# Performance work log

Hardware: AMD Instinct MI355X
Metric: run time of the kernel (lower is better)

Reference implementation:

```python
import jax, jax.numpy as jnp
import numpy as np

N = 100000      # nodes
E = 3200000     # edges (avg degree 32)
DIN = 128       # in_channels
DH = 256        # hidden == out_channels


def _xavier(key, fan_in, fan_out):
    s = float(np.sqrt(2.0 / (fan_in + fan_out)))
    return jax.random.normal(key, (fan_in, fan_out), dtype=jnp.float32) * s


def setup_inputs() -> dict:
    key = jax.random.key(0)
    ks = jax.random.split(key, 16)
    x = jax.random.normal(ks[0], (N, DIN), dtype=jnp.float32)
    edge_index = jax.random.randint(ks[1], (2, E), 0, N, dtype=jnp.int32)
    inp = {"x": x, "edge_index": edge_index}
    dims = [(DIN, DH), (DH, DH), (DH, DH), (DH, DH), (DH, DH), (DH, DH)]
    names = [("w11", "b11"), ("w12", "b12"), ("w21", "b21"), ("w22", "b22"), ("w31", "b31"), ("w32", "b32")]
    for i, ((di, do), (wn, bn)) in enumerate(zip(dims, names)):
        inp[wn] = _xavier(ks[2 + i], di, do)
        inp[bn] = jnp.zeros((do,), dtype=jnp.float32)
    return inp


def reference(x, edge_index, w11, b11, w12, b12, w21, b21, w22, b22, w31, b31, w32, b32):
    src, dst = edge_index[0], edge_index[1]

    def gin_conv(h, w1, b1, w2, b2):
        # sum-aggregate neighbor features: agg[i] = sum_{(j->i) in E} h[j]
        agg = jax.ops.segment_sum(h[src], dst, num_segments=N)
        h2 = h + agg                      # (1 + eps) * x + agg, eps = 0
        h2 = jax.nn.relu(h2 @ w1 + b1)    # mlp layer 1
        return h2 @ w2 + b2               # mlp layer 2 (no activation)

    h = jax.nn.relu(gin_conv(x, w11, b11, w12, b12))
    h = jax.nn.relu(gin_conv(h, w21, b21, w22, b22))
    return gin_conv(h, w31, b31, w32, b32)
```

## Files before the change

kernel.cpp:

```cpp
#include <hip/hip_runtime.h>
#include <hip/hip_bf16.h>
#include <hip/hip_fp16.h>


#define DIN 128
#define DH  256
#define BM  256
#define BN  128
#define BK  64

#define BSHIFT 9
#define BNODES 512
#define MAXB   256
#define PBLK   256

__global__ __launch_bounds__(1024) void k_bhist(const int* __restrict__ dst,
                                                int* __restrict__ cntMat,
                                                int E, int nbuck, int chunk) {
    __shared__ int h[MAXB];
    for (int i = threadIdx.x; i < nbuck; i += 1024) h[i] = 0;
    __syncthreads();
    const int b = blockIdx.x;
    const int lo = b * chunk, hi = min(lo + chunk, E);
    for (int i = lo + (int)threadIdx.x; i < hi; i += 1024)
        atomicAdd(&h[dst[i] >> BSHIFT], 1);
    __syncthreads();
    for (int i = threadIdx.x; i < nbuck; i += 1024) cntMat[b * nbuck + i] = h[i];
}

__global__ __launch_bounds__(256) void k_bscan(const int* __restrict__ cntMat,
                                               int* __restrict__ bbase,
                                               int* __restrict__ baseMat,
                                               int nbuck, int E) {
    __shared__ int tot[MAXB];
    __shared__ int base[MAXB + 1];
    const int k = threadIdx.x;
    if (k < nbuck) {
        int s = 0;
        for (int b = 0; b < PBLK; ++b) s += cntMat[b * nbuck + k];
        tot[k] = s;
    }
    __syncthreads();
    if (k == 0) {
        int acc = 0;
        for (int i = 0; i < nbuck; ++i) { base[i] = acc; acc += tot[i]; }
        base[nbuck] = acc;
    }
    __syncthreads();
    if (k < nbuck) {
        bbase[k] = base[k];
        int acc = base[k];
        for (int b = 0; b < PBLK; ++b) { baseMat[b * nbuck + k] = acc; acc += cntMat[b * nbuck + k]; }
    }
    if (k == 0) bbase[nbuck] = E;
}

__global__ __launch_bounds__(1024) void k_bpart(const int* __restrict__ src,
                                                const int* __restrict__ dst,
                                                const int* __restrict__ baseMat,
                                                uint2* __restrict__ pairb,
                                                int E, int nbuck, int chunk) {
    __shared__ int cur[MAXB];
    const int b = blockIdx.x;
    for (int i = threadIdx.x; i < nbuck; i += 1024) cur[i] = baseMat[b * nbuck + i];
    __syncthreads();
    const int lo = b * chunk, hi = min(lo + chunk, E);
    for (int i = lo + (int)threadIdx.x; i < hi; i += 1024) {
        int d = dst[i], s = src[i];
        int pos = atomicAdd(&cur[d >> BSHIFT], 1);
        pairb[pos] = make_uint2((unsigned)d, (unsigned)s);
    }
}

__global__ __launch_bounds__(1024) void k_bcsr(const uint2* __restrict__ pairb,
                                               const int* __restrict__ bbase,
                                               int* __restrict__ rp,
                                               int* __restrict__ csr,
                                               int N, int E) {
    __shared__ int cnt[BNODES];
    __shared__ int cur[BNODES];
    const int k = blockIdx.x;
    const int node0 = k << BSHIFT;
    const int nn = min(BNODES, N - node0);
    const int lo = bbase[k], hi = bbase[k + 1];
    const int tid = threadIdx.x;

    for (int i = tid; i < BNODES; i += 1024) cnt[i] = 0;
    __syncthreads();
    for (int i = lo + tid; i < hi; i += 1024)
        atomicAdd(&cnt[pairb[i].x - node0], 1);
    __syncthreads();

    int v = 0;
    if (tid < BNODES) { v = cnt[tid]; cur[tid] = v; }
    __syncthreads();
    for (int off = 1; off < BNODES; off <<= 1) {
        int add = (tid < BNODES && tid >= off) ? cur[tid - off] : 0;
        __syncthreads();
        if (tid < BNODES) cur[tid] += add;
        __syncthreads();
    }
    if (tid < nn) {
        int start = lo + cur[tid] - v;
        rp[node0 + tid] = start;
        cur[tid] = start;
    }
    __syncthreads();
    for (int i = lo + tid; i < hi; i += 1024) {
        uint2 e = pairb[i];
        int pos = atomicAdd(&cur[e.x - node0], 1);
        csr[pos] = (int)e.y;
    }
    if (k == 0 && tid == 0) rp[N] = E;
}

struct PrepArgs {
    const float* W[6];
    __half* Wh[6];
    const float* x;
    __half* xh;
};

__global__ __launch_bounds__(256) void k_prep(PrepArgs a, int n4) {
    int bid = blockIdx.x;
    if (bid < 1408) {
        int w, local;
        if (bid < 128) { w = 0; local = bid; }
        else { w = 1 + (bid - 128) / 256; local = (bid - 128) & 255; }
        const int K = (w == 0) ? DIN : DH;
        int idx = local * 256 + (int)threadIdx.x;
        int k = idx >> 8, c = idx & 255;
        a.Wh[w][c * K + k] = __float2half(a.W[w][idx]);
    } else {
        int i = (bid - 1408) * 256 + (int)threadIdx.x;
        if (i >= n4) return;
        float4 f = *(const float4*)(a.x + (size_t)i * 4);
        __half2 h0 = __floats2half2_rn(f.x, f.y);
        __half2 h1 = __floats2half2_rn(f.z, f.w);
        uint2 o;
        o.x = __builtin_bit_cast(unsigned, h0);
        o.y = __builtin_bit_cast(unsigned, h1);
        *(uint2*)(a.xh + (size_t)i * 4) = o;
    }
}

__device__ __forceinline__ void addrow4(unsigned lo, unsigned hi,
                                        float& a0, float& a1, float& a2, float& a3) {
    __half2 h0 = __builtin_bit_cast(__half2, lo);
    __half2 h1 = __builtin_bit_cast(__half2, hi);
    float2 f0 = __half22float2(h0);
    float2 f1 = __half22float2(h1);
    a0 += f0.x; a1 += f0.y; a2 += f1.x; a3 += f1.y;
}

__global__ __launch_bounds__(256) void k_aggh256(const __half* __restrict__ H,
                                                 const int* __restrict__ rp,
                                                 const int* __restrict__ csr,
                                                 __half* __restrict__ out, int n) {
    int node = (int)((blockIdx.x * 256 + threadIdx.x) >> 6);
    if (node >= n) return;
    int lane = threadIdx.x & 63;
    const size_t lo4 = (size_t)lane * 4;
    float a0, a1, a2, a3;
    {
        uint2 v = *(const uint2*)(H + (size_t)node * DH + lo4);
        a0 = a1 = a2 = a3 = 0.f;
        addrow4(v.x, v.y, a0, a1, a2, a3);
    }
    int p = rp[node], pe = rp[node + 1];
    for (; p + 3 < pe; p += 4) {
        int j0 = csr[p], j1 = csr[p + 1], j2 = csr[p + 2], j3 = csr[p + 3];
        uint2 v0 = *(const uint2*)(H + (size_t)j0 * DH + lo4);
        uint2 v1 = *(const uint2*)(H + (size_t)j1 * DH + lo4);
        uint2 v2 = *(const uint2*)(H + (size_t)j2 * DH + lo4);
        uint2 v3 = *(const uint2*)(H + (size_t)j3 * DH + lo4);
        addrow4(v0.x, v0.y, a0, a1, a2, a3);
        addrow4(v1.x, v1.y, a0, a1, a2, a3);
        addrow4(v2.x, v2.y, a0, a1, a2, a3);
        addrow4(v3.x, v3.y, a0, a1, a2, a3);
    }
    for (; p < pe; ++p) {
        uint2 v = *(const uint2*)(H + (size_t)csr[p] * DH + lo4);
        addrow4(v.x, v.y, a0, a1, a2, a3);
    }
    __half2 o0 = __floats2half2_rn(a0, a1);
    __half2 o1 = __floats2half2_rn(a2, a3);
    uint2 ov;
    ov.x = __builtin_bit_cast(unsigned, o0);
    ov.y = __builtin_bit_cast(unsigned, o1);
    *(uint2*)(out + (size_t)node * DH + lo4) = ov;
}

__global__ __launch_bounds__(256) void k_aggh128(const __half* __restrict__ H,
                                                 const int* __restrict__ rp,
                                                 const int* __restrict__ csr,
                                                 __half* __restrict__ out, int n) {
    int node = (int)((blockIdx.x * 256 + threadIdx.x) >> 6);
    if (node >= n) return;
    int lane = threadIdx.x & 63;
    const size_t lo2 = (size_t)lane * 2;
    float a0, a1;
    {
        unsigned v = *(const unsigned*)(H + (size_t)node * DIN + lo2);
        float2 f = __half22float2(__builtin_bit_cast(__half2, v));
        a0 = f.x; a1 = f.y;
    }
    int p = rp[node], pe = rp[node + 1];
    for (; p + 3 < pe; p += 4) {
        int j0 = csr[p], j1 = csr[p + 1], j2 = csr[p + 2], j3 = csr[p + 3];
        unsigned v0 = *(const unsigned*)(H + (size_t)j0 * DIN + lo2);
        unsigned v1 = *(const unsigned*)(H + (size_t)j1 * DIN + lo2);
        unsigned v2 = *(const unsigned*)(H + (size_t)j2 * DIN + lo2);
        unsigned v3 = *(const unsigned*)(H + (size_t)j3 * DIN + lo2);
        float2 f0 = __half22float2(__builtin_bit_cast(__half2, v0));
        float2 f1 = __half22float2(__builtin_bit_cast(__half2, v1));
        float2 f2 = __half22float2(__builtin_bit_cast(__half2, v2));
        float2 f3 = __half22float2(__builtin_bit_cast(__half2, v3));
        a0 += f0.x + f1.x + f2.x + f3.x;
        a1 += f0.y + f1.y + f2.y + f3.y;
    }
    for (; p < pe; ++p) {
        unsigned v = *(const unsigned*)(H + (size_t)csr[p] * DIN + lo2);
        float2 f = __half22float2(__builtin_bit_cast(__half2, v));
        a0 += f.x; a1 += f.y;
    }
    __half2 o = __floats2half2_rn(a0, a1);
    *(unsigned*)(out + (size_t)node * DIN + lo2) = __builtin_bit_cast(unsigned, o);
}

typedef __attribute__((ext_vector_type(8))) _Float16 f16x8;
typedef __attribute__((ext_vector_type(4))) float     f32x4;

template<int K, int MODE>
__global__ __launch_bounds__(256, 2) void k_gemm_mfma(
        const __half* __restrict__ A,
        const __half* __restrict__ Wt,
        const float* __restrict__ bias,
        void* __restrict__ Cout, int M) {
    __shared__ __align__(16) __half As[BM * BK];
    __shared__ __align__(16) __half Ws[BN * BK];

    const int t    = threadIdx.x;
    const int lane = t & 63;
    const int wid  = t >> 6;
    const int wr   = wid >> 1;
    const int wc   = wid & 1;
    const int brow = (int)blockIdx.x * BM;
    const int bcol = (int)blockIdx.y * BN;

    f32x4 acc[8][4] = {};

    for (int k0 = 0; k0 < K; k0 += BK) {
#pragma unroll
        for (int i = 0; i < 8; ++i) {
            int idx = i * 256 + t;
            int r = idx >> 3, q = idx & 7;
            uint4 v = *(const uint4*)(A + (size_t)(brow + r) * K + k0 + q * 8);
            *(uint4*)((char*)As + r * 128 + ((q ^ (r & 7)) << 4)) = v;
        }
#pragma unroll
        for (int i = 0; i < 4; ++i) {
            int idx = i * 256 + t;
            int c = idx >> 3, q = idx & 7;
            uint4 vh = *(const uint4*)(Wt + (size_t)(bcol + c) * K + k0 + q * 8);
            *(uint4*)((char*)Ws + c * 128 + ((q ^ (c & 7)) << 4)) = vh;
        }
        __syncthreads();

#pragma unroll
        for (int kk = 0; kk < 2; ++kk) {
            const int qa = kk * 4 + (lane >> 4);
            f16x8 af[8], wf[4];
#pragma unroll
            for (int mi = 0; mi < 8; ++mi) {
                int r = wr * 128 + mi * 16 + (lane & 15);
                af[mi] = *(const f16x8*)((const char*)As + r * 128 + ((qa ^ (r & 7)) << 4));
            }
#pragma unroll
            for (int ni = 0; ni < 4; ++ni) {
                int c = wc * 64 + ni * 16 + (lane & 15);
                wf[ni] = *(const f16x8*)((const char*)Ws + c * 128 + ((qa ^ (c & 7)) << 4));
            }
#pragma unroll
            for (int mi = 0; mi < 8; ++mi)
#pragma unroll
                for (int ni = 0; ni < 4; ++ni)
                    acc[mi][ni] = __builtin_amdgcn_mfma_f32_16x16x32_f16(af[mi], wf[ni], acc[mi][ni], 0, 0, 0);
        }
        __syncthreads();
    }

#pragma unroll
    for (int ni = 0; ni < 4; ++ni) {
        const int c = bcol + wc * 64 + ni * 16 + (lane & 15);
        const float bz = bias[c];
#pragma unroll
        for (int mi = 0; mi < 8; ++mi) {
            const int r0 = brow + wr * 128 + mi * 16 + ((lane >> 4) << 2);
#pragma unroll
            for (int j = 0; j < 4; ++j) {
                int row = r0 + j;
                if (row < M) {
                    float v = acc[mi][ni][j] + bz;
                    if (MODE == 0) {
                        v = fmaxf(v, 0.f);
                        ((__half*)Cout)[(size_t)row * DH + c] = __float2half(v);
                    } else {
                        ((float*)Cout)[(size_t)row * DH + c] = v;
                    }
                }
            }
        }
    }
}

static inline size_t align256(size_t x) { return (x + 255) & ~(size_t)255; }

extern "C" void kernel_launch(void* const* d_in, const int* in_sizes, int n_in,
                              void* d_out, int out_size, void* d_ws, size_t ws_size,
                              hipStream_t stream) {
    const float* x   = (const float*)d_in[0];
    const int*   ei  = (const int*)d_in[1];
    const float* W[6]  = {(const float*)d_in[2], (const float*)d_in[4],
                          (const float*)d_in[6], (const float*)d_in[8],
                          (const float*)d_in[10], (const float*)d_in[12]};
    const float* Bv[6] = {(const float*)d_in[3], (const float*)d_in[5],
                          (const float*)d_in[7], (const float*)d_in[9],
                          (const float*)d_in[11], (const float*)d_in[13]};

    const int N = in_sizes[0] / DIN;
    const int E = in_sizes[1] / 2;
    const int Mpad = ((N + BM - 1) / BM) * BM;
    const int* src = ei;
    const int* dst = ei + E;
    const int nbuck  = (N + BNODES - 1) / BNODES;
    const int chunkE = (E + PBLK - 1) / PBLK;

    char* ws = (char*)d_ws;
    __half* A1 = (__half*)ws; ws += align256((size_t)Mpad * DIN * 2);
    __half* Ah = (__half*)ws; ws += align256((size_t)Mpad * DH * 2);
    __half* T  = (__half*)ws; ws += align256((size_t)Mpad * DH * 2);
    __half* Hh = (__half*)ws; ws += align256((size_t)Mpad * DH * 2);
    __half* Xh = (__half*)T;
    uint2* pairb = (uint2*)Ah;
    __half* Wh[6];
    const int Ks[6] = {DIN, DH, DH, DH, DH, DH};
    for (int i = 0; i < 6; ++i) {
        Wh[i] = (__half*)ws; ws += align256((size_t)Ks[i] * DH * 2);
    }
    int* cntMat  = (int*)ws; ws += align256((size_t)PBLK * MAXB * 4);
    int* baseMat = (int*)ws; ws += align256((size_t)PBLK * MAXB * 4);
    int* bbase   = (int*)ws; ws += align256((size_t)(MAXB + 1) * 4);
    int* rp      = (int*)ws; ws += align256((size_t)(N + 1) * 4);
    int* csr     = (int*)ws; ws += align256((size_t)E * 4);
    float* O = (float*)d_out;

    PrepArgs pa;
    for (int i = 0; i < 6; ++i) { pa.W[i] = W[i]; pa.Wh[i] = Wh[i]; }
    pa.x = x; pa.xh = Xh;
    const int n4 = N * DIN / 4;
    const int castBlocks = (n4 + 255) / 256;
    k_prep<<<1408 + castBlocks, 256, 0, stream>>>(pa, n4);

    k_bhist<<<PBLK, 1024, 0, stream>>>(dst, cntMat, E, nbuck, chunkE);
    k_bscan<<<1, 256, 0, stream>>>(cntMat, bbase, baseMat, nbuck, E);
    k_bpart<<<PBLK, 1024, 0, stream>>>(src, dst, baseMat, pairb, E, nbuck, chunkE);
    k_bcsr<<<nbuck, 1024, 0, stream>>>(pairb, bbase, rp, csr, N, E);

    const int gAgg = (N + 3) / 4;
    dim3 gGemm(Mpad / BM, DH / BN);

    k_aggh128<<<gAgg, 256, 0, stream>>>(Xh, rp, csr, A1, N);
    k_gemm_mfma<DIN, 0><<<gGemm, 256, 0, stream>>>(A1, Wh[0], Bv[0], T, N);
    k_gemm_mfma<DH,  0><<<gGemm, 256, 0, stream>>>(T,  Wh[1], Bv[1], Hh, N);
    k_aggh256<<<gAgg, 256, 0, stream>>>(Hh, rp, csr, Ah, N);
    k_gemm_mfma<DH,  0><<<gGemm, 256, 0, stream>>>(Ah, Wh[2], Bv[2], T, N);
    k_gemm_mfma<DH,  0><<<gGemm, 256, 0, stream>>>(T,  Wh[3], Bv[3], Hh, N);
    k_aggh256<<<gAgg, 256, 0, stream>>>(Hh, rp, csr, Ah, N);
    k_gemm_mfma<DH,  0><<<gGemm, 256, 0, stream>>>(Ah, Wh[4], Bv[4], T, N);
    k_gemm_mfma<DH,  1><<<gGemm, 256, 0, stream>>>(T,  Wh[5], Bv[5], O, N);
}
```

Measured before the change: 1.134 ms.

## Split hidden features into two column planes for cache-friendly aggregation

The second-layer GEMM now writes its 256-wide fp16 output as two separate 128-column planes. Each aggregation pass then gathers from one 25.6MB plane instead of the full 51MB array, so the gathered working set fits better in L2/MALL. The cost is twice as many aggregation launches, a second read of the CSR index arrays per layer, and narrower 4-byte gathers per lane.

```diff
diff --git a/kernel.cpp b/kernel.cpp
--- a/kernel.cpp
+++ b/kernel.cpp
@@ -144,74 +144,28 @@
     }
 }
 
-__device__ __forceinline__ void addrow4(unsigned lo, unsigned hi,
-                                        float& a0, float& a1, float& a2, float& a3) {
-    __half2 h0 = __builtin_bit_cast(__half2, lo);
-    __half2 h1 = __builtin_bit_cast(__half2, hi);
-    float2 f0 = __half22float2(h0);
-    float2 f1 = __half22float2(h1);
-    a0 += f0.x; a1 += f0.y; a2 += f1.x; a3 += f1.y;
-}
-
-__global__ __launch_bounds__(256) void k_aggh256(const __half* __restrict__ H,
-                                                 const int* __restrict__ rp,
-                                                 const int* __restrict__ csr,
-                                                 __half* __restrict__ out, int n) {
+__global__ __launch_bounds__(256) void k_aggp(const __half* __restrict__ Hp,
+                                              const int* __restrict__ rp,
+                                              const int* __restrict__ csr,
+                                              __half* __restrict__ out,
+                                              int outStride, int outOff, int n) {
     int node = (int)((blockIdx.x * 256 + threadIdx.x) >> 6);
     if (node >= n) return;
     int lane = threadIdx.x & 63;
-    const size_t lo4 = (size_t)lane * 4;
-    float a0, a1, a2, a3;
+    const __half* Hl = Hp + (size_t)lane * 2;
+    float a0, a1;
     {
-        uint2 v = *(const uint2*)(H + (size_t)node * DH + lo4);
-        a0 = a1 = a2 = a3 = 0.f;
-        addrow4(v.x, v.y, a0, a1, a2, a3);
+        unsigned v = *(const unsigned*)(Hl + (size_t)node * 128);
+        float2 f = __half22float2(__builtin_bit_cast(__half2, v));
+        a0 = f.x; a1 = f.y;
     }
     int p = rp[node], pe = rp[node + 1];
     for (; p + 3 < pe; p += 4) {
         int j0 = csr[p], j1 = csr[p + 1], j2 = csr[p + 2], j3 = csr[p + 3];
-        uint2 v0 = *(const uint2*)(H + (size_t)j0 * DH + lo4);
-        uint2 v1 = *(const uint2*)(H + (size_t)j1 * DH + lo4);
-        uint2 v2 = *(const uint2*)(H + (size_t)j2 * DH + lo4);
-        uint2 v3 = *(const uint2*)(H + (size_t)j3 * DH + lo4);
-        addrow4(v0.x, v0.y, a0, a1, a2, a3);
-        addrow4(v1.x, v1.y, a0, a1, a2, a3);
-        addrow4(v2.x, v2.y, a0, a1, a2, a3);
-        addrow4(v3.x, v3.y, a0, a1, a2, a3);
-    }
-    for (; p < pe; ++p) {
-        uint2 v = *(const uint2*)(H + (size_t)csr[p] * DH + lo4);
-        addrow4(v.x, v.y, a0, a1, a2, a3);
-    }
-    __half2 o0 = __floats2half2_rn(a0, a1);
-    __half2 o1 = __floats2half2_rn(a2, a3);
-    uint2 ov;
-    ov.x = __builtin_bit_cast(unsigned, o0);
-    ov.y = __builtin_bit_cast(unsigned, o1);
-    *(uint2*)(out + (size_t)node * DH + lo4) = ov;
-}
-
-__global__ __launch_bounds__(256) void k_aggh128(const __half* __restrict__ H,
-                                                 const int* __restrict__ rp,
-                                                 const int* __restrict__ csr,
-                                                 __half* __restrict__ out, int n) {
-    int node = (int)((blockIdx.x * 256 + threadIdx.x) >> 6);
-    if (node >= n) return;
-    int lane = threadIdx.x & 63;
-    const size_t lo2 = (size_t)lane * 2;
-    float a0, a1;
-    {
-        unsigned v = *(const unsigned*)(H + (size_t)node * DIN + lo2);
-        float2 f = __half22float2(__builtin_bit_cast(__half2, v));
-        a0 = f.x; a1 = f.y;
-    }
-    int p = rp[node], pe = rp[node + 1];
-    for (; p + 3 < pe; p += 4) {
-        int j0 = csr[p], j1 = csr[p + 1], j2 = csr[p + 2], j3 = csr[p + 3];
-        unsigned v0 = *(const unsigned*)(H + (size_t)j0 * DIN + lo2);
-        unsigned v1 = *(const unsigned*)(H + (size_t)j1 * DIN + lo2);
-        unsigned v2 = *(const unsigned*)(H + (size_t)j2 * DIN + lo2);
-        unsigned v3 = *(const unsigned*)(H + (size_t)j3 * DIN + lo2);
+        unsigned v0 = *(const unsigned*)(Hl + (size_t)j0 * 128);
+        unsigned v1 = *(const unsigned*)(Hl + (size_t)j1 * 128);
+        unsigned v2 = *(const unsigned*)(Hl + (size_t)j2 * 128);
+        unsigned v3 = *(const unsigned*)(Hl + (size_t)j3 * 128);
         float2 f0 = __half22float2(__builtin_bit_cast(__half2, v0));
         float2 f1 = __half22float2(__builtin_bit_cast(__half2, v1));
         float2 f2 = __half22float2(__builtin_bit_cast(__half2, v2));
@@ -220,12 +174,13 @@
         a1 += f0.y + f1.y + f2.y + f3.y;
     }
     for (; p < pe; ++p) {
-        unsigned v = *(const unsigned*)(H + (size_t)csr[p] * DIN + lo2);
+        unsigned v = *(const unsigned*)(Hl + (size_t)csr[p] * 128);
         float2 f = __half22float2(__builtin_bit_cast(__half2, v));
         a0 += f.x; a1 += f.y;
     }
     __half2 o = __floats2half2_rn(a0, a1);
-    *(unsigned*)(out + (size_t)node * DIN + lo2) = __builtin_bit_cast(unsigned, o);
+    *(unsigned*)(out + (size_t)node * outStride + outOff + (size_t)lane * 2) =
+        __builtin_bit_cast(unsigned, o);
 }
 
 typedef __attribute__((ext_vector_type(8))) _Float16 f16x8;
@@ -236,7 +191,7 @@
         const __half* __restrict__ A,
         const __half* __restrict__ Wt,
         const float* __restrict__ bias,
-        void* __restrict__ Cout, int M) {
+        void* __restrict__ Cout, void* __restrict__ Cout2, int M) {
     __shared__ __align__(16) __half As[BM * BK];
     __shared__ __align__(16) __half Ws[BN * BK];
 
@@ -290,9 +245,11 @@
         __syncthreads();
     }
 
+    __half* Plane = (__half*)(blockIdx.y == 0 ? Cout : Cout2);
 #pragma unroll
     for (int ni = 0; ni < 4; ++ni) {
-        const int c = bcol + wc * 64 + ni * 16 + (lane & 15);
+        const int cl = wc * 64 + ni * 16 + (lane & 15);
+        const int c  = bcol + cl;
         const float bz = bias[c];
 #pragma unroll
         for (int mi = 0; mi < 8; ++mi) {
@@ -305,8 +262,11 @@
                     if (MODE == 0) {
                         v = fmaxf(v, 0.f);
                         ((__half*)Cout)[(size_t)row * DH + c] = __float2half(v);
+                    } else if (MODE == 1) {
+                        ((float*)Cout)[(size_t)row * DH + c] = v;
                     } else {
-                        ((float*)Cout)[(size_t)row * DH + c] = v;
+                        v = fmaxf(v, 0.f);
+                        Plane[(size_t)row * 128 + cl] = __float2half(v);
                     }
                 }
             }
@@ -337,10 +297,11 @@
     const int chunkE = (E + PBLK - 1) / PBLK;
 
     char* ws = (char*)d_ws;
-    __half* A1 = (__half*)ws; ws += align256((size_t)Mpad * DIN * 2);
-    __half* Ah = (__half*)ws; ws += align256((size_t)Mpad * DH * 2);
-    __half* T  = (__half*)ws; ws += align256((size_t)Mpad * DH * 2);
-    __half* Hh = (__half*)ws; ws += align256((size_t)Mpad * DH * 2);
+    __half* A1  = (__half*)ws; ws += align256((size_t)Mpad * DIN * 2);
+    __half* Ah  = (__half*)ws; ws += align256((size_t)Mpad * DH * 2);
+    __half* T   = (__half*)ws; ws += align256((size_t)Mpad * DH * 2);
+    __half* Hp0 = (__half*)ws; ws += align256((size_t)Mpad * 128 * 2);
+    __half* Hp1 = (__half*)ws; ws += align256((size_t)Mpad * 128 * 2);
     __half* Xh = (__half*)T;
     uint2* pairb = (uint2*)Ah;
     __half* Wh[6];
@@ -370,13 +331,15 @@
     const int gAgg = (N + 3) / 4;
     dim3 gGemm(Mpad / BM, DH / BN);
 
-    k_aggh128<<<gAgg, 256, 0, stream>>>(Xh, rp, csr, A1, N);
-    k_gemm_mfma<DIN, 0><<<gGemm, 256, 0, stream>>>(A1, Wh[0], Bv[0], T, N);
-    k_gemm_mfma<DH,  0><<<gGemm, 256, 0, stream>>>(T,  Wh[1], Bv[1], Hh, N);
-    k_aggh256<<<gAgg, 256, 0, stream>>>(Hh, rp, csr, Ah, N);
-    k_gemm_mfma<DH,  0><<<gGemm, 256, 0, stream>>>(Ah, Wh[2], Bv[2], T, N);
-    k_gemm_mfma<DH,  0><<<gGemm, 256, 0, stream>>>(T,  Wh[3], Bv[3], Hh, N);
-    k_aggh256<<<gAgg, 256, 0, stream>>>(Hh, rp, csr, Ah, N);
-    k_gemm_mfma<DH,  0><<<gGemm, 256, 0, stream>>>(Ah, Wh[4], Bv[4], T, N);
-    k_gemm_mfma<DH,  1><<<gGemm, 256, 0, stream>>>(T,  Wh[5], Bv[5], O, N);
-}
+    k_aggp<<<gAgg, 256, 0, stream>>>(Xh, rp, csr, A1, 128, 0, N);
+    k_gemm_mfma<DIN, 0><<<gGemm, 256, 0, stream>>>(A1, Wh[0], Bv[0], T, nullptr, N);
+    k_gemm_mfma<DH,  2><<<gGemm, 256, 0, stream>>>(T,  Wh[1], Bv[1], Hp0, Hp1, N);
+    k_aggp<<<gAgg, 256, 0, stream>>>(Hp0, rp, csr, Ah, 256, 0,   N);
+    k_aggp<<<gAgg, 256, 0, stream>>>(Hp1, rp, csr, Ah, 256, 128, N);
+    k_gemm_mfma<DH,  0><<<gGemm, 256, 0, stream>>>(Ah, Wh[2], Bv[2], T, nullptr, N);
+    k_gemm_mfma<DH,  2><<<gGemm, 256, 0, stream>>>(T,  Wh[3], Bv[3], Hp0, Hp1, N);
+    k_aggp<<<gAgg, 256, 0, stream>>>(Hp0, rp, csr, Ah, 256, 0,   N);
+    k_aggp<<<gAgg, 256, 0, stream>>>(Hp1, rp, csr, Ah, 256, 128, N);
+    k_gemm_mfma<DH,  0><<<gGemm, 256, 0, stream>>>(Ah, Wh[4], Bv[4], T, nullptr, N);
+    k_gemm_mfma<DH,  1><<<gGemm, 256, 0, stream>>>(T,  Wh[5], Bv[5], O, nullptr, N);
+}
```

New measurement: 1.168 ms. 1.03x slower.
